# Kernel tuning notes

Hardware: AMD Instinct MI355X
Metric: run time of the kernel (lower is better)

## Reference

```python
import jax, jax.numpy as jnp
import numpy as np

N_NODES = 100000
N_EDGES = 1600000
F_IN = 128
HID = 64
N_CLASSES = 1
N_GRAPHS = 1024


def gcn_conv(x, src, dst, deg_inv_sqrt, W, b):
    # PyG GCNConv: out = D^{-1/2}(A+I)D^{-1/2} X W + b
    xw = x @ W  # [N, H]
    norm = deg_inv_sqrt[src] * deg_inv_sqrt[dst]  # [E]
    msg = xw[src] * norm[:, None]  # gather + scale
    agg = jax.ops.segment_sum(msg, dst, num_segments=N_NODES)
    # self-loop contribution: norm_ii = deg_inv_sqrt[i]^2
    agg = agg + xw * (deg_inv_sqrt ** 2)[:, None]
    return agg + b


def setup_inputs() -> dict:
    key = jax.random.key(0)
    ks = jax.random.split(key, 12)
    x = jax.random.normal(ks[0], (N_NODES, F_IN), dtype=jnp.float32)
    edge_index = jax.random.randint(ks[1], (2, N_EDGES), 0, N_NODES, dtype=jnp.int64)
    batch = jnp.sort(jax.random.randint(ks[2], (N_NODES,), 0, N_GRAPHS, dtype=jnp.int64))
    def glorot(k, fan_in, fan_out):
        s = (6.0 / (fan_in + fan_out)) ** 0.5
        return jax.random.uniform(k, (fan_in, fan_out), dtype=jnp.float32, minval=-s, maxval=s)
    W1 = glorot(ks[3], F_IN, HID); b1 = jnp.zeros((HID,), jnp.float32)
    W2 = glorot(ks[4], HID, HID); b2 = jnp.zeros((HID,), jnp.float32)
    W3 = glorot(ks[5], HID, HID); b3 = jnp.zeros((HID,), jnp.float32)
    Wl = glorot(ks[6], HID, N_CLASSES); bl = jnp.zeros((N_CLASSES,), jnp.float32)
    return {"x": x, "edge_index": edge_index, "batch": batch,
            "W1": W1, "b1": b1, "W2": W2, "b2": b2, "W3": W3, "b3": b3,
            "Wl": Wl, "bl": bl}


def reference(x, edge_index, batch, W1, b1, W2, b2, W3, b3, Wl, bl):
    src, dst = edge_index[0], edge_index[1]
    # degree with self-loops: deg[i] = (# incoming edges at i) + 1
    deg = jax.ops.segment_sum(jnp.ones((N_EDGES,), x.dtype), dst, num_segments=N_NODES) + 1.0
    deg_inv_sqrt = jax.lax.rsqrt(deg)
    h = jax.nn.relu(gcn_conv(x, src, dst, deg_inv_sqrt, W1, b1))
    # dropout: identity in eval mode
    h = jax.nn.relu(gcn_conv(h, src, dst, deg_inv_sqrt, W2, b2))
    h = gcn_conv(h, src, dst, deg_inv_sqrt, W3, b3)
    # global_mean_pool over graph ids
    sums = jax.ops.segment_sum(h, batch, num_segments=N_GRAPHS)
    counts = jax.ops.segment_sum(jnp.ones((N_NODES,), h.dtype), batch, num_segments=N_GRAPHS)
    pooled = sums / jnp.maximum(counts, 1.0)[:, None]  # [G, HID]
    return pooled @ Wl + bl  # [G, num_classes]
```

## Files before the change

### kernel.cpp

```cpp
#include <hip/hip_runtime.h>
#include <hip/hip_bf16.h>

#define N_NODES 100000
#define N_EDGES 1600000
#define F_IN 128
#define HID 64
#define N_GRAPHS 1024

#define SH 9
#define NBU 196
#define NB 200
#define BCAP 9728
#define EPB 2048
#define NSLICE 2

typedef __attribute__((ext_vector_type(8))) short bf16x8;
typedef __attribute__((ext_vector_type(4))) float f32x4;
typedef __attribute__((ext_vector_type(4))) unsigned int u32x4;

__device__ __forceinline__ unsigned short f2bf(float f) {
    __hip_bfloat16 h = __float2bfloat16(f);
    return *reinterpret_cast<unsigned short*>(&h);
}
__device__ __forceinline__ float bf2f(unsigned int u) {
    return __uint_as_float(u << 16);
}

__device__ __forceinline__ float loadf(const void* p, size_t i, int f32) {
    if (f32) return ((const float*)p)[i];
    return __bfloat162float(((const __hip_bfloat16*)p)[i]);
}
__device__ __forceinline__ int loadi(const void* p, size_t i, int i64) {
    if (i64) return (int)((const long long*)p)[i];
    return ((const int*)p)[i];
}

__global__ void k_init(const unsigned int* __restrict__ xw_,
                       const unsigned int* __restrict__ ei_,
                       int* __restrict__ flags,
                       int* __restrict__ gcnt, int* __restrict__ bcnt) {
    __shared__ int cnt_f, cnt_i;
    int t = threadIdx.x;
    if (t == 0) { cnt_f = 0; cnt_i = 0; }
    __syncthreads();
    unsigned int w = xw_[t];
    unsigned int e = (w >> 7) & 0xFFu;
    if (e >= 100u && e <= 140u) atomicAdd(&cnt_f, 1);
    unsigned int iw = ei_[2 * t + 1];
    if (iw == 0u) atomicAdd(&cnt_i, 1);
    for (int i = t; i < N_GRAPHS; i += 256) gcnt[i] = 0;
    for (int i = t; i < NB; i += 256) bcnt[i] = 0;
    __syncthreads();
    if (t == 0) {
        flags[0] = (cnt_f < 180) ? 1 : 0;
        flags[1] = (cnt_i >= 128) ? 1 : 0;
    }
}

__global__ __launch_bounds__(256) void k_part(const void* __restrict__ ei,
                                              const void* __restrict__ batch,
                                              int* __restrict__ bcnt,
                                              int* __restrict__ gcnt,
                                              unsigned int* __restrict__ packed,
                                              const int* __restrict__ flags) {
    int I64 = flags[1];
    __shared__ int hist[NB];
    __shared__ int base[NB];
    __shared__ int ghist[N_GRAPHS];
    __shared__ unsigned int elds[EPB];
    __shared__ unsigned char ebkt[EPB];
    int t = threadIdx.x;
    if (t < NB) hist[t] = 0;
    for (int i = t; i < N_GRAPHS; i += 256) ghist[i] = 0;
    __syncthreads();
    if (t < 128) {
        int n = blockIdx.x * 128 + t;
        if (n < N_NODES) atomicAdd(&ghist[loadi(batch, n, I64)], 1);
    }
    int e0 = blockIdx.x * EPB;
#pragma unroll 4
    for (int it = 0; it < EPB / 256; ++it) {
        int idx = it * 256 + t;
        int e = e0 + idx;
        unsigned int pv = 0u;
        unsigned char bk = 0xFFu;
        if (e < N_EDGES) {
            int sN = loadi(ei, e, I64);
            int d = loadi(ei, (size_t)N_EDGES + e, I64);
            bk = (unsigned char)(d >> SH);
            pv = ((unsigned int)sN << SH) | (unsigned int)(d & 511);
            atomicAdd(&hist[d >> SH], 1);
        }
        elds[idx] = pv;
        ebkt[idx] = bk;
    }
    __syncthreads();
    if (t < NB) {
        base[t] = hist[t] ? atomicAdd(&bcnt[t], hist[t]) : 0;
        hist[t] = 0;
    }
    for (int i = t; i < N_GRAPHS; i += 256)
        if (ghist[i]) atomicAdd(&gcnt[i], ghist[i]);
    __syncthreads();
#pragma unroll 4
    for (int it = 0; it < EPB / 256; ++it) {
        int idx = it * 256 + t;
        unsigned char bk = ebkt[idx];
        if (bk != 0xFFu) {
            unsigned int pv = elds[idx];
            int r = atomicAdd(&hist[bk], 1);
            int pos = base[bk] + r;
            if (pos < BCAP)
                packed[(size_t)bk * BCAP + pos] = pv;
        }
    }
}

__global__ __launch_bounds__(512) void k_csr(const unsigned int* __restrict__ packed,
                                             const int* __restrict__ bcnt,
                                             float* __restrict__ dis,
                                             int2* __restrict__ rp2,
                                             int* __restrict__ csr,
                                             const int* __restrict__ gcnt,
                                             int* __restrict__ gptr) {
    __shared__ int hist[512];
    __shared__ int offs[512];
    __shared__ int elds[BCAP];
    int b = blockIdx.x;
    int t = threadIdx.x;
    if (b == NBU) {
        int a = gcnt[2 * t], bq = gcnt[2 * t + 1];
        int ps = a + bq;
        hist[t] = ps;
        __syncthreads();
        for (int off = 1; off < 512; off <<= 1) {
            int x = (t >= off) ? hist[t - off] : 0;
            __syncthreads();
            hist[t] += x;
            __syncthreads();
        }
        int excl = hist[t] - ps;
        gptr[2 * t] = excl;
        gptr[2 * t + 1] = excl + a;
        if (t == 511) gptr[1024] = hist[511];
        return;
    }
    int n = bcnt[b]; if (n > BCAP) n = BCAP;
    hist[t] = 0;
    __syncthreads();
    const unsigned int* pb = packed + (size_t)b * BCAP;
    for (int i = t; i < n; i += 512)
        atomicAdd(&hist[pb[i] & 511u], 1);
    __syncthreads();
    int c = hist[t];
    offs[t] = c;
    __syncthreads();
    for (int off = 1; off < 512; off <<= 1) {
        int x = (t >= off) ? offs[t - off] : 0;
        __syncthreads();
        offs[t] += x;
        __syncthreads();
    }
    int excl = offs[t] - c;
    int node = (b << SH) + t;
    int base = b * BCAP;
    if (node < N_NODES) {
        dis[node] = rsqrtf((float)c + 1.0f);
        rp2[node] = make_int2(base + excl, base + excl + c);
    }
    __syncthreads();
    offs[t] = excl;
    __syncthreads();
    for (int i = t; i < n; i += 512) {
        unsigned int p = pb[i];
        int pos = atomicAdd(&offs[p & 511u], 1);
        if (pos < BCAP) elds[pos] = (int)(p >> SH);
    }
    __syncthreads();
    for (int i = t; i < n; i += 512)
        csr[base + i] = elds[i];
}

template <int K>
__global__ __launch_bounds__(256) void k_gemm(const void* __restrict__ x,
                                              const void* __restrict__ W,
                                              const float* __restrict__ dis,
                                              unsigned short* __restrict__ out,
                                              const int* __restrict__ flags,
                                              int x_is_f32) {
    int Wf32 = flags[0];
    int xF32 = (x_is_f32 < 0) ? Wf32 : x_is_f32;
    __shared__ unsigned short Wt[64][K + 8];
    __shared__ unsigned short xs[32][K + 8];
    int t = threadIdx.x;
    int wave = t >> 6, lane = t & 63;
    int quad = lane >> 4, l16 = lane & 15;

    for (int id = t; id < 64 * K; id += 256) {
        int k = id >> 6, n = id & 63;
        Wt[n][k] = f2bf(loadf(W, id, Wf32));
    }
    __syncthreads();

    bf16x8 bfrag[K / 32];
#pragma unroll
    for (int c = 0; c < K / 32; ++c)
        bfrag[c] = *reinterpret_cast<bf16x8*>(&Wt[wave * 16 + l16][c * 32 + quad * 8]);

    const int ngroups = (N_NODES + 31) / 32;
    for (int g = blockIdx.x; g < ngroups; g += gridDim.x) {
        __syncthreads();
        int row0 = g * 32;
        for (int cid = t; cid < 4 * K; cid += 256) {
            int rr = cid / (K / 8), c8 = cid % (K / 8);
            int r = row0 + rr;
            u32x4 val = {0u, 0u, 0u, 0u};
            if (r < N_NODES) {
                size_t base = (size_t)r * K + c8 * 8;
                if (xF32) {
                    const u32x4* xp = (const u32x4*)x;
                    u32x4 q0 = xp[base / 4];
                    u32x4 q1 = xp[base / 4 + 1];
                    val.x = f2bf(__uint_as_float(q0.x)) | ((unsigned int)f2bf(__uint_as_float(q0.y)) << 16);
                    val.y = f2bf(__uint_as_float(q0.z)) | ((unsigned int)f2bf(__uint_as_float(q0.w)) << 16);
                    val.z = f2bf(__uint_as_float(q1.x)) | ((unsigned int)f2bf(__uint_as_float(q1.y)) << 16);
                    val.w = f2bf(__uint_as_float(q1.z)) | ((unsigned int)f2bf(__uint_as_float(q1.w)) << 16);
                } else {
                    val = ((const u32x4*)x)[base / 8];
                }
            }
            *reinterpret_cast<u32x4*>(&xs[rr][c8 * 8]) = val;
        }
        __syncthreads();

        f32x4 acc0 = {0.f, 0.f, 0.f, 0.f};
        f32x4 acc1 = {0.f, 0.f, 0.f, 0.f};
#pragma unroll
        for (int c = 0; c < K / 32; ++c) {
            bf16x8 a0 = *reinterpret_cast<bf16x8*>(&xs[l16][c * 32 + quad * 8]);
            bf16x8 a1 = *reinterpret_cast<bf16x8*>(&xs[16 + l16][c * 32 + quad * 8]);
            acc0 = __builtin_amdgcn_mfma_f32_16x16x32_bf16(a0, bfrag[c], acc0, 0, 0, 0);
            acc1 = __builtin_amdgcn_mfma_f32_16x16x32_bf16(a1, bfrag[c], acc1, 0, 0, 0);
        }
        int col = wave * 16 + l16;
        unsigned short* ow = out + (size_t)(col >> 5) * (N_NODES * 32);
        int f = col & 31;
#pragma unroll
        for (int reg = 0; reg < 4; ++reg) {
            int r0 = row0 + quad * 4 + reg;
            if (r0 < N_NODES) ow[(size_t)r0 * 32 + f] = f2bf(acc0[reg] * dis[r0]);
            int r1 = row0 + 16 + quad * 4 + reg;
            if (r1 < N_NODES) ow[(size_t)r1 * 32 + f] = f2bf(acc1[reg] * dis[r1]);
        }
    }
}

__global__ __launch_bounds__(256) void k_gather_sm(const int2* __restrict__ rp2,
                                                   const int* __restrict__ csr,
                                                   const float* __restrict__ dis,
                                                   const unsigned short* __restrict__ xws,
                                                   const void* __restrict__ bias,
                                                   unsigned short* __restrict__ out,
                                                   const int* __restrict__ flags) {
    int F32 = flags[0];
    int blk = blockIdx.x;
    int xcd = blk & 7;
    int s = xcd >> 2;
    int grp = ((blk >> 3) << 2) | (xcd & 3);
    int wave = threadIdx.x >> 6, lane = threadIdx.x & 63;
    int nodesub = lane >> 4;
    int eslot = (lane >> 2) & 3;
    int q = lane & 3;
    const u32x4* xs4 = (const u32x4*)(xws + (size_t)s * N_NODES * 32);
    u32x4* op = (u32x4*)out;
    float bb0 = loadf(bias, s * 32 + q * 8 + 0, F32);
    float bb1 = loadf(bias, s * 32 + q * 8 + 1, F32);
    float bb2 = loadf(bias, s * 32 + q * 8 + 2, F32);
    float bb3 = loadf(bias, s * 32 + q * 8 + 3, F32);
    float bb4 = loadf(bias, s * 32 + q * 8 + 4, F32);
    float bb5 = loadf(bias, s * 32 + q * 8 + 5, F32);
    float bb6 = loadf(bias, s * 32 + q * 8 + 6, F32);
    float bb7 = loadf(bias, s * 32 + q * 8 + 7, F32);
    int wbase = grp * 64 + wave * 16;

    for (int ni = 0; ni < 4; ++ni) {
        int node = wbase + ni * 4 + nodesub;
        int valid = node < N_NODES;
        int2 se = valid ? rp2[node] : make_int2(0, 0);
        float a0 = 0.f, a1 = 0.f, a2 = 0.f, a3 = 0.f;
        float a4 = 0.f, a5 = 0.f, a6 = 0.f, a7 = 0.f;
        int j = se.x + eslot;
        if (j < se.y) {
            int src = csr[j];
            u32x4 vc = xs4[(size_t)src * 4 + q];
            int jn = j + 4;
            int sn = (jn < se.y) ? csr[jn] : 0;
            while (jn < se.y) {
                u32x4 vn = xs4[(size_t)sn * 4 + q];
                int jn2 = jn + 4;
                int sn2 = (jn2 < se.y) ? csr[jn2] : 0;
                a0 += bf2f(vc.x & 0xFFFFu); a1 += bf2f(vc.x >> 16);
                a2 += bf2f(vc.y & 0xFFFFu); a3 += bf2f(vc.y >> 16);
                a4 += bf2f(vc.z & 0xFFFFu); a5 += bf2f(vc.z >> 16);
                a6 += bf2f(vc.w & 0xFFFFu); a7 += bf2f(vc.w >> 16);
                vc = vn; sn = sn2; jn = jn2;
            }
            a0 += bf2f(vc.x & 0xFFFFu); a1 += bf2f(vc.x >> 16);
            a2 += bf2f(vc.y & 0xFFFFu); a3 += bf2f(vc.y >> 16);
            a4 += bf2f(vc.z & 0xFFFFu); a5 += bf2f(vc.z >> 16);
            a6 += bf2f(vc.w & 0xFFFFu); a7 += bf2f(vc.w >> 16);
        }
#pragma unroll
        for (int off = 4; off <= 8; off <<= 1) {
            a0 += __shfl_down(a0, off, 64); a1 += __shfl_down(a1, off, 64);
            a2 += __shfl_down(a2, off, 64); a3 += __shfl_down(a3, off, 64);
            a4 += __shfl_down(a4, off, 64); a5 += __shfl_down(a5, off, 64);
            a6 += __shfl_down(a6, off, 64); a7 += __shfl_down(a7, off, 64);
        }
        if (((lane & 12) == 0) && valid) {
            u32x4 sv = xs4[(size_t)node * 4 + q];
            float dn = dis[node];
            float v0 = fmaf(a0 + bf2f(sv.x & 0xFFFFu), dn, bb0);
            float v1 = fmaf(a1 + bf2f(sv.x >> 16),     dn, bb1);
            float v2 = fmaf(a2 + bf2f(sv.y & 0xFFFFu), dn, bb2);
            float v3 = fmaf(a3 + bf2f(sv.y >> 16),     dn, bb3);
            float v4 = fmaf(a4 + bf2f(sv.z & 0xFFFFu), dn, bb4);
            float v5 = fmaf(a5 + bf2f(sv.z >> 16),     dn, bb5);
            float v6 = fmaf(a6 + bf2f(sv.w & 0xFFFFu), dn, bb6);
            float v7 = fmaf(a7 + bf2f(sv.w >> 16),     dn, bb7);
            v0 = fmaxf(v0, 0.f) * dn; v1 = fmaxf(v1, 0.f) * dn;
            v2 = fmaxf(v2, 0.f) * dn; v3 = fmaxf(v3, 0.f) * dn;
            v4 = fmaxf(v4, 0.f) * dn; v5 = fmaxf(v5, 0.f) * dn;
            v6 = fmaxf(v6, 0.f) * dn; v7 = fmaxf(v7, 0.f) * dn;
            u32x4 o;
            o.x = (unsigned int)f2bf(v0) | ((unsigned int)f2bf(v1) << 16);
            o.y = (unsigned int)f2bf(v2) | ((unsigned int)f2bf(v3) << 16);
            o.z = (unsigned int)f2bf(v4) | ((unsigned int)f2bf(v5) << 16);
            o.w = (unsigned int)f2bf(v6) | ((unsigned int)f2bf(v7) << 16);
            op[(size_t)node * 8 + s * 4 + q] = o;
        }
    }
}

__global__ __launch_bounds__(256) void k_fgl(const int2* __restrict__ rp2,
                                             const int* __restrict__ csr,
                                             const float* __restrict__ dis,
                                             const unsigned short* __restrict__ hs_in,
                                             const void* __restrict__ W,
                                             const void* __restrict__ bias,
                                             unsigned short* __restrict__ out,
                                             int relu_scale,
                                             const int* __restrict__ flags) {
    int F32 = flags[0];
    __shared__ unsigned short Wt[64][72];
    __shared__ unsigned short xs[64][72];
    int t = threadIdx.x;
    int w = t >> 6, lane = t & 63;
    for (int id = t; id < 64 * 64; id += 256) {
        int k = id >> 6, n = id & 63;
        Wt[n][k] = f2bf(loadf(W, id, F32));
    }
    int node2 = lane >> 5;
    int oct = lane & 7;
    const u32x4* xr = (const u32x4*)hs_in;
    int wbase = blockIdx.x * 64 + w * 16;
#pragma unroll
    for (int p = 0; p < 8; ++p) {
        int node = wbase + p * 2 + node2;
        int valid = node < N_NODES;
        int2 se = valid ? rp2[node] : make_int2(0, 0);
        float a0 = 0.f, a1 = 0.f, a2 = 0.f, a3 = 0.f;
        float a4 = 0.f, a5 = 0.f, a6 = 0.f, a7 = 0.f;
        int j = se.x + ((lane >> 3) & 3);
        if (j < se.y) {
            int src = csr[j];
            u32x4 vc = xr[(size_t)src * 8 + oct];
            int jn = j + 4;
            int sn = (jn < se.y) ? csr[jn] : 0;
            while (jn < se.y) {
                u32x4 vn = xr[(size_t)sn * 8 + oct];
                int jn2 = jn + 4;
                int sn2 = (jn2 < se.y) ? csr[jn2] : 0;
                a0 += bf2f(vc.x & 0xFFFFu); a1 += bf2f(vc.x >> 16);
                a2 += bf2f(vc.y & 0xFFFFu); a3 += bf2f(vc.y >> 16);
                a4 += bf2f(vc.z & 0xFFFFu); a5 += bf2f(vc.z >> 16);
                a6 += bf2f(vc.w & 0xFFFFu); a7 += bf2f(vc.w >> 16);
                vc = vn; sn = sn2; jn = jn2;
            }
            a0 += bf2f(vc.x & 0xFFFFu); a1 += bf2f(vc.x >> 16);
            a2 += bf2f(vc.y & 0xFFFFu); a3 += bf2f(vc.y >> 16);
            a4 += bf2f(vc.z & 0xFFFFu); a5 += bf2f(vc.z >> 16);
            a6 += bf2f(vc.w & 0xFFFFu); a7 += bf2f(vc.w >> 16);
        }
#pragma unroll
        for (int off = 8; off <= 16; off <<= 1) {
            a0 += __shfl_down(a0, off, 64); a1 += __shfl_down(a1, off, 64);
            a2 += __shfl_down(a2, off, 64); a3 += __shfl_down(a3, off, 64);
            a4 += __shfl_down(a4, off, 64); a5 += __shfl_down(a5, off, 64);
            a6 += __shfl_down(a6, off, 64); a7 += __shfl_down(a7, off, 64);
        }
        if ((lane & 24) == 0) {
            u32x4 sv = {0u, 0u, 0u, 0u};
            float dn = 0.f;
            if (valid) { sv = xr[(size_t)node * 8 + oct]; dn = dis[node]; }
            float v0 = (a0 + bf2f(sv.x & 0xFFFFu)) * dn;
            float v1 = (a1 + bf2f(sv.x >> 16))     * dn;
            float v2 = (a2 + bf2f(sv.y & 0xFFFFu)) * dn;
            float v3 = (a3 + bf2f(sv.y >> 16))     * dn;
            float v4 = (a4 + bf2f(sv.z & 0xFFFFu)) * dn;
            float v5 = (a5 + bf2f(sv.z >> 16))     * dn;
            float v6 = (a6 + bf2f(sv.w & 0xFFFFu)) * dn;
            float v7 = (a7 + bf2f(sv.w >> 16))     * dn;
            u32x4 o;
            o.x = (unsigned int)f2bf(v0) | ((unsigned int)f2bf(v1) << 16);
            o.y = (unsigned int)f2bf(v2) | ((unsigned int)f2bf(v3) << 16);
            o.z = (unsigned int)f2bf(v4) | ((unsigned int)f2bf(v5) << 16);
            o.w = (unsigned int)f2bf(v6) | ((unsigned int)f2bf(v7) << 16);
            *reinterpret_cast<u32x4*>(&xs[w * 16 + p * 2 + node2][oct * 8]) = o;
        }
    }
    __syncthreads();
    int quad = lane >> 4, l16 = lane & 15;
    bf16x8 bfrag[2];
#pragma unroll
    for (int c = 0; c < 2; ++c)
        bfrag[c] = *reinterpret_cast<bf16x8*>(&Wt[w * 16 + l16][c * 32 + quad * 8]);
    f32x4 acc[4];
#pragma unroll
    for (int rg = 0; rg < 4; ++rg) acc[rg] = (f32x4){0.f, 0.f, 0.f, 0.f};
#pragma unroll
    for (int c = 0; c < 2; ++c) {
#pragma unroll
        for (int rg = 0; rg < 4; ++rg) {
            bf16x8 a = *reinterpret_cast<bf16x8*>(&xs[rg * 16 + l16][c * 32 + quad * 8]);
            acc[rg] = __builtin_amdgcn_mfma_f32_16x16x32_bf16(a, bfrag[c], acc[rg], 0, 0, 0);
        }
    }
    int col = w * 16 + l16;
    float bcol = loadf(bias, col, F32);
    int rbase = blockIdx.x * 64;
#pragma unroll
    for (int rg = 0; rg < 4; ++rg) {
#pragma unroll
        for (int reg = 0; reg < 4; ++reg) {
            int row = rbase + rg * 16 + quad * 4 + reg;
            if (row < N_NODES) {
                float v = acc[rg][reg] + bcol;
                if (relu_scale) v = fmaxf(v, 0.f) * dis[row];
                out[(size_t)row * 64 + col] = f2bf(v);
            }
        }
    }
}

__global__ __launch_bounds__(256) void k_pool3(const int* __restrict__ gptr,
                                               const int2* __restrict__ rp2,
                                               const int* __restrict__ csr,
                                               const float* __restrict__ dis,
                                               const unsigned short* __restrict__ hs,
                                               const void* __restrict__ W3,
                                               const void* __restrict__ b3,
                                               const void* __restrict__ Wl,
                                               const void* __restrict__ bl,
                                               void* __restrict__ out,
                                               const int* __restrict__ flags) {
    int F32 = flags[0];
    __shared__ float w3l[64];
    __shared__ float part[4];
    __shared__ float cterm;
    int t = threadIdx.x;
    if (t < 64) {
        float acc = 0.f;
        for (int k = 0; k < 64; ++k)
            acc += loadf(W3, t * 64 + k, F32) * loadf(Wl, k, F32);
        w3l[t] = acc;
    }
    if (t == 64) {
        float acc = 0.f;
        for (int k = 0; k < 64; ++k)
            acc += loadf(b3, k, F32) * loadf(Wl, k, F32);
        cterm = acc;
    }
    __syncthreads();
    int g = blockIdx.x;
    int w = t >> 6, lane = t & 63;
    int eslot = lane >> 3, oct = lane & 7;
    int s0 = gptr[g], e0 = gptr[g + 1];
    const u32x4* xr = (const u32x4*)hs;
    float P0 = 0.f, P1 = 0.f, P2 = 0.f, P3 = 0.f;
    float P4 = 0.f, P5 = 0.f, P6 = 0.f, P7 = 0.f;
    for (int node = s0 + w; node < e0; node += 4) {
        int2 se = rp2[node];
        float t0 = 0.f, t1 = 0.f, t2 = 0.f, t3 = 0.f;
        float t4 = 0.f, t5 = 0.f, t6 = 0.f, t7 = 0.f;
        int j = se.x + eslot;
        if (j < se.y) {
            int src = csr[j];
            u32x4 vc = xr[(size_t)src * 8 + oct];
            int jn = j + 8;
            int sn = (jn < se.y) ? csr[jn] : 0;
            while (jn < se.y) {
                u32x4 vn = xr[(size_t)sn * 8 + oct];
                int jn2 = jn + 8;
                int sn2 = (jn2 < se.y) ? csr[jn2] : 0;
                t0 += bf2f(vc.x & 0xFFFFu); t1 += bf2f(vc.x >> 16);
                t2 += bf2f(vc.y & 0xFFFFu); t3 += bf2f(vc.y >> 16);
                t4 += bf2f(vc.z & 0xFFFFu); t5 += bf2f(vc.z >> 16);
                t6 += bf2f(vc.w & 0xFFFFu); t7 += bf2f(vc.w >> 16);
                vc = vn; sn = sn2; jn = jn2;
            }
            t0 += bf2f(vc.x & 0xFFFFu); t1 += bf2f(vc.x >> 16);
            t2 += bf2f(vc.y & 0xFFFFu); t3 += bf2f(vc.y >> 16);
            t4 += bf2f(vc.z & 0xFFFFu); t5 += bf2f(vc.z >> 16);
            t6 += bf2f(vc.w & 0xFFFFu); t7 += bf2f(vc.w >> 16);
        }
        if (eslot == 0) {
            u32x4 sv = xr[(size_t)node * 8 + oct];
            t0 += bf2f(sv.x & 0xFFFFu); t1 += bf2f(sv.x >> 16);
            t2 += bf2f(sv.y & 0xFFFFu); t3 += bf2f(sv.y >> 16);
            t4 += bf2f(sv.z & 0xFFFFu); t5 += bf2f(sv.z >> 16);
            t6 += bf2f(sv.w & 0xFFFFu); t7 += bf2f(sv.w >> 16);
        }
        float dn = dis[node];
        P0 = fmaf(t0, dn, P0); P1 = fmaf(t1, dn, P1);
        P2 = fmaf(t2, dn, P2); P3 = fmaf(t3, dn, P3);
        P4 = fmaf(t4, dn, P4); P5 = fmaf(t5, dn, P5);
        P6 = fmaf(t6, dn, P6); P7 = fmaf(t7, dn, P7);
    }
#pragma unroll
    for (int off = 8; off <= 32; off <<= 1) {
        P0 += __shfl_down(P0, off, 64); P1 += __shfl_down(P1, off, 64);
        P2 += __shfl_down(P2, off, 64); P3 += __shfl_down(P3, off, 64);
        P4 += __shfl_down(P4, off, 64); P5 += __shfl_down(P5, off, 64);
        P6 += __shfl_down(P6, off, 64); P7 += __shfl_down(P7, off, 64);
    }
    float v = 0.f;
    if (eslot == 0) {
        int f = oct * 8;
        v = P0 * w3l[f] + P1 * w3l[f + 1] + P2 * w3l[f + 2] + P3 * w3l[f + 3]
          + P4 * w3l[f + 4] + P5 * w3l[f + 5] + P6 * w3l[f + 6] + P7 * w3l[f + 7];
    }
    v += __shfl_down(v, 4, 64);
    v += __shfl_down(v, 2, 64);
    v += __shfl_down(v, 1, 64);
    if (lane == 0) part[w] = v;
    __syncthreads();
    if (t == 0) {
        float cnt = fmaxf((float)(e0 - s0), 1.0f);
        float r = (part[0] + part[1] + part[2] + part[3]) / cnt
                + ((e0 > s0) ? cterm : 0.f) + loadf(bl, 0, F32);
        if (F32) ((float*)out)[g] = r;
        else     ((__hip_bfloat16*)out)[g] = __float2bfloat16(r);
    }
}

extern "C" void kernel_launch(void* const* d_in, const int* in_sizes, int n_in,
                              void* d_out, int out_size, void* d_ws, size_t ws_size,
                              hipStream_t stream) {
    const void* x     = d_in[0];
    const void* ei    = d_in[1];
    const void* batch = d_in[2];
    const void* W1 = d_in[3];
    const void* b1 = d_in[4];
    const void* W2 = d_in[5];
    const void* b2 = d_in[6];
    const void* W3 = d_in[7];
    const void* b3 = d_in[8];
    const void* Wl = d_in[9];
    const void* bl = d_in[10];

    float* dis   = (float*)d_ws;
    int2*  rp2   = (int2*)(dis + 100352);
    int*   csr   = (int*)(rp2 + 100352);
    int*   gcnt  = csr + NB * BCAP;
    int*   gptr  = gcnt + 1024;
    int*   bcnt  = gptr + 1056;
    int*   flags = bcnt + 256;
    unsigned int* packed = (unsigned int*)(flags + 16);
    unsigned short* bufA = (unsigned short*)(packed + (size_t)NB * BCAP);
    unsigned short* bufB = bufA + (size_t)N_NODES * 64;

    const int TB = 256;
    dim3 blk(TB);
    int gGA = 391 * 8;
    int gFG = (N_NODES + 63) / 64;

    k_init<<<1, blk, 0, stream>>>((const unsigned int*)x, (const unsigned int*)ei,
                                  flags, gcnt, bcnt);
    k_part<<<(N_EDGES + EPB - 1) / EPB, blk, 0, stream>>>(ei, batch, bcnt, gcnt, packed, flags);
    k_csr<<<NBU + 1, 512, 0, stream>>>(packed, bcnt, dis, rp2, csr, gcnt, gptr);

    k_gemm<F_IN><<<1024, blk, 0, stream>>>(x, W1, dis, bufA, flags, -1);
    k_gather_sm<<<gGA, blk, 0, stream>>>(rp2, csr, dis, bufA, b1, bufB, flags);
    k_fgl<<<gFG, blk, 0, stream>>>(rp2, csr, dis, bufB, W2, b2, bufA, 1, flags);
    k_pool3<<<N_GRAPHS, blk, 0, stream>>>(gptr, rp2, csr, dis, bufA,
                                          W3, b3, Wl, bl, d_out, flags);
}
```

Baseline: 342.3 us.

## Project layer-3 features to scalars before aggregation and pool with atomics

Layer 3 and the head are linear, so each node's 64-wide feature is first reduced to one scalar z = h·(W3·Wl). Aggregation then gathers scalars instead of 64-wide bf16 rows, and graph pooling uses float atomics into a per-graph accumulator. The W3·Wl product moves into the init kernel. This cuts layer-3 gather traffic by about 64x, at the cost of two extra launches and atomic contention on graph sums; atomic ordering also makes the float summation non-deterministic.

```diff
diff --git a/kernel.cpp b/kernel.cpp
--- a/kernel.cpp
+++ b/kernel.cpp
@@ -38,8 +38,11 @@
 __global__ void k_init(const unsigned int* __restrict__ xw_,
                        const unsigned int* __restrict__ ei_,
                        int* __restrict__ flags,
-                       int* __restrict__ gcnt, int* __restrict__ bcnt) {
-    __shared__ int cnt_f, cnt_i;
+                       int* __restrict__ gcnt, int* __restrict__ bcnt,
+                       const void* __restrict__ W3, const void* __restrict__ b3,
+                       const void* __restrict__ Wl,
+                       float* __restrict__ w3l, float* __restrict__ gacc) {
+    __shared__ int cnt_f, cnt_i, sF32;
     int t = threadIdx.x;
     if (t == 0) { cnt_f = 0; cnt_i = 0; }
     __syncthreads();
@@ -48,12 +51,28 @@
     if (e >= 100u && e <= 140u) atomicAdd(&cnt_f, 1);
     unsigned int iw = ei_[2 * t + 1];
     if (iw == 0u) atomicAdd(&cnt_i, 1);
-    for (int i = t; i < N_GRAPHS; i += 256) gcnt[i] = 0;
+    for (int i = t; i < N_GRAPHS; i += 256) { gcnt[i] = 0; gacc[i] = 0.f; }
     for (int i = t; i < NB; i += 256) bcnt[i] = 0;
     __syncthreads();
     if (t == 0) {
-        flags[0] = (cnt_f < 180) ? 1 : 0;
+        int f = (cnt_f < 180) ? 1 : 0;
+        flags[0] = f;
         flags[1] = (cnt_i >= 128) ? 1 : 0;
+        sF32 = f;
+    }
+    __syncthreads();
+    int F32 = sF32;
+    if (t < 64) {
+        float acc = 0.f;
+        for (int k = 0; k < 64; ++k)
+            acc += loadf(W3, t * 64 + k, F32) * loadf(Wl, k, F32);
+        w3l[t] = acc;
+    }
+    if (t == 64) {
+        float acc = 0.f;
+        for (int k = 0; k < 64; ++k)
+            acc += loadf(b3, k, F32) * loadf(Wl, k, F32);
+        w3l[64] = acc;
     }
 }
 
@@ -453,105 +472,67 @@
     }
 }
 
-__global__ __launch_bounds__(256) void k_pool3(const int* __restrict__ gptr,
-                                               const int2* __restrict__ rp2,
-                                               const int* __restrict__ csr,
-                                               const float* __restrict__ dis,
-                                               const unsigned short* __restrict__ hs,
-                                               const void* __restrict__ W3,
-                                               const void* __restrict__ b3,
-                                               const void* __restrict__ Wl,
-                                               const void* __restrict__ bl,
-                                               void* __restrict__ out,
-                                               const int* __restrict__ flags) {
+__global__ __launch_bounds__(256) void k_z(const unsigned short* __restrict__ hs,
+                                           const float* __restrict__ w3l,
+                                           float* __restrict__ z) {
+    __shared__ float w3s[64];
+    int t = threadIdx.x;
+    if (t < 64) w3s[t] = w3l[t];
+    __syncthreads();
+    int lane = t & 63, wave = t >> 6;
+    int rowsub = lane >> 3, oct = lane & 7;
+    int node = blockIdx.x * 32 + wave * 8 + rowsub;
+    const u32x4* xr = (const u32x4*)hs;
+    u32x4 v = xr[(size_t)node * 8 + oct];
+    int f = oct * 8;
+    float pd = bf2f(v.x & 0xFFFFu) * w3s[f + 0] + bf2f(v.x >> 16) * w3s[f + 1]
+             + bf2f(v.y & 0xFFFFu) * w3s[f + 2] + bf2f(v.y >> 16) * w3s[f + 3]
+             + bf2f(v.z & 0xFFFFu) * w3s[f + 4] + bf2f(v.z >> 16) * w3s[f + 5]
+             + bf2f(v.w & 0xFFFFu) * w3s[f + 6] + bf2f(v.w >> 16) * w3s[f + 7];
+    pd += __shfl_down(pd, 4, 64);
+    pd += __shfl_down(pd, 2, 64);
+    pd += __shfl_down(pd, 1, 64);
+    if (oct == 0) z[node] = pd;
+}
+
+__global__ __launch_bounds__(256) void k_l3(const int2* __restrict__ rp2,
+                                            const int* __restrict__ csr,
+                                            const float* __restrict__ dis,
+                                            const float* __restrict__ z,
+                                            const void* __restrict__ batch,
+                                            float* __restrict__ gacc,
+                                            const int* __restrict__ flags) {
+    int I64 = flags[1];
+    int node = blockIdx.x * 256 + threadIdx.x;
+    if (node >= N_NODES) return;
+    int2 se = rp2[node];
+    float sum = z[node];
+    int j = se.x;
+    if (j < se.y) {
+        int s = csr[j];
+        for (;;) {
+            int jn = j + 1;
+            int sn = (jn < se.y) ? csr[jn] : 0;
+            sum += z[s];
+            if (jn >= se.y) break;
+            j = jn; s = sn;
+        }
+    }
+    float y = dis[node] * sum;
+    unsafeAtomicAdd(&gacc[loadi(batch, node, I64)], y);
+}
+
+__global__ void k_head(const int* __restrict__ gptr, const float* __restrict__ gacc,
+                       const float* __restrict__ w3l, const void* __restrict__ bl,
+                       void* __restrict__ out, const int* __restrict__ flags) {
     int F32 = flags[0];
-    __shared__ float w3l[64];
-    __shared__ float part[4];
-    __shared__ float cterm;
-    int t = threadIdx.x;
-    if (t < 64) {
-        float acc = 0.f;
-        for (int k = 0; k < 64; ++k)
-            acc += loadf(W3, t * 64 + k, F32) * loadf(Wl, k, F32);
-        w3l[t] = acc;
-    }
-    if (t == 64) {
-        float acc = 0.f;
-        for (int k = 0; k < 64; ++k)
-            acc += loadf(b3, k, F32) * loadf(Wl, k, F32);
-        cterm = acc;
-    }
-    __syncthreads();
-    int g = blockIdx.x;
-    int w = t >> 6, lane = t & 63;
-    int eslot = lane >> 3, oct = lane & 7;
-    int s0 = gptr[g], e0 = gptr[g + 1];
-    const u32x4* xr = (const u32x4*)hs;
-    float P0 = 0.f, P1 = 0.f, P2 = 0.f, P3 = 0.f;
-    float P4 = 0.f, P5 = 0.f, P6 = 0.f, P7 = 0.f;
-    for (int node = s0 + w; node < e0; node += 4) {
-        int2 se = rp2[node];
-        float t0 = 0.f, t1 = 0.f, t2 = 0.f, t3 = 0.f;
-        float t4 = 0.f, t5 = 0.f, t6 = 0.f, t7 = 0.f;
-        int j = se.x + eslot;
-        if (j < se.y) {
-            int src = csr[j];
-            u32x4 vc = xr[(size_t)src * 8 + oct];
-            int jn = j + 8;
-            int sn = (jn < se.y) ? csr[jn] : 0;
-            while (jn < se.y) {
-                u32x4 vn = xr[(size_t)sn * 8 + oct];
-                int jn2 = jn + 8;
-                int sn2 = (jn2 < se.y) ? csr[jn2] : 0;
-                t0 += bf2f(vc.x & 0xFFFFu); t1 += bf2f(vc.x >> 16);
-                t2 += bf2f(vc.y & 0xFFFFu); t3 += bf2f(vc.y >> 16);
-                t4 += bf2f(vc.z & 0xFFFFu); t5 += bf2f(vc.z >> 16);
-                t6 += bf2f(vc.w & 0xFFFFu); t7 += bf2f(vc.w >> 16);
-                vc = vn; sn = sn2; jn = jn2;
-            }
-            t0 += bf2f(vc.x & 0xFFFFu); t1 += bf2f(vc.x >> 16);
-            t2 += bf2f(vc.y & 0xFFFFu); t3 += bf2f(vc.y >> 16);
-            t4 += bf2f(vc.z & 0xFFFFu); t5 += bf2f(vc.z >> 16);
-            t6 += bf2f(vc.w & 0xFFFFu); t7 += bf2f(vc.w >> 16);
-        }
-        if (eslot == 0) {
-            u32x4 sv = xr[(size_t)node * 8 + oct];
-            t0 += bf2f(sv.x & 0xFFFFu); t1 += bf2f(sv.x >> 16);
-            t2 += bf2f(sv.y & 0xFFFFu); t3 += bf2f(sv.y >> 16);
-            t4 += bf2f(sv.z & 0xFFFFu); t5 += bf2f(sv.z >> 16);
-            t6 += bf2f(sv.w & 0xFFFFu); t7 += bf2f(sv.w >> 16);
-        }
-        float dn = dis[node];
-        P0 = fmaf(t0, dn, P0); P1 = fmaf(t1, dn, P1);
-        P2 = fmaf(t2, dn, P2); P3 = fmaf(t3, dn, P3);
-        P4 = fmaf(t4, dn, P4); P5 = fmaf(t5, dn, P5);
-        P6 = fmaf(t6, dn, P6); P7 = fmaf(t7, dn, P7);
-    }
-#pragma unroll
-    for (int off = 8; off <= 32; off <<= 1) {
-        P0 += __shfl_down(P0, off, 64); P1 += __shfl_down(P1, off, 64);
-        P2 += __shfl_down(P2, off, 64); P3 += __shfl_down(P3, off, 64);
-        P4 += __shfl_down(P4, off, 64); P5 += __shfl_down(P5, off, 64);
-        P6 += __shfl_down(P6, off, 64); P7 += __shfl_down(P7, off, 64);
-    }
-    float v = 0.f;
-    if (eslot == 0) {
-        int f = oct * 8;
-        v = P0 * w3l[f] + P1 * w3l[f + 1] + P2 * w3l[f + 2] + P3 * w3l[f + 3]
-          + P4 * w3l[f + 4] + P5 * w3l[f + 5] + P6 * w3l[f + 6] + P7 * w3l[f + 7];
-    }
-    v += __shfl_down(v, 4, 64);
-    v += __shfl_down(v, 2, 64);
-    v += __shfl_down(v, 1, 64);
-    if (lane == 0) part[w] = v;
-    __syncthreads();
-    if (t == 0) {
-        float cnt = fmaxf((float)(e0 - s0), 1.0f);
-        float r = (part[0] + part[1] + part[2] + part[3]) / cnt
-                + ((e0 > s0) ? cterm : 0.f) + loadf(bl, 0, F32);
-        if (F32) ((float*)out)[g] = r;
-        else     ((__hip_bfloat16*)out)[g] = __float2bfloat16(r);
-    }
+    int g = blockIdx.x * 256 + threadIdx.x;
+    if (g >= N_GRAPHS) return;
+    int cnt = gptr[g + 1] - gptr[g];
+    float r = (cnt > 0) ? (gacc[g] / (float)cnt + w3l[64]) : 0.f;
+    r += loadf(bl, 0, F32);
+    if (F32) ((float*)out)[g] = r;
+    else     ((__hip_bfloat16*)out)[g] = __float2bfloat16(r);
 }
 
 extern "C" void kernel_launch(void* const* d_in, const int* in_sizes, int n_in,
@@ -576,7 +557,10 @@
     int*   gptr  = gcnt + 1024;
     int*   bcnt  = gptr + 1056;
     int*   flags = bcnt + 256;
-    unsigned int* packed = (unsigned int*)(flags + 16);
+    float* w3l   = (float*)(flags + 16);
+    float* gacc  = w3l + 80;
+    unsigned int* packed = (unsigned int*)(gacc + 1024);
+    float* z = (float*)packed;
     unsigned short* bufA = (unsigned short*)(packed + (size_t)NB * BCAP);
     unsigned short* bufB = bufA + (size_t)N_NODES * 64;
 
@@ -586,13 +570,14 @@
     int gFG = (N_NODES + 63) / 64;
 
     k_init<<<1, blk, 0, stream>>>((const unsigned int*)x, (const unsigned int*)ei,
-                                  flags, gcnt, bcnt);
+                                  flags, gcnt, bcnt, W3, b3, Wl, w3l, gacc);
     k_part<<<(N_EDGES + EPB - 1) / EPB, blk, 0, stream>>>(ei, batch, bcnt, gcnt, packed, flags);
     k_csr<<<NBU + 1, 512, 0, stream>>>(packed, bcnt, dis, rp2, csr, gcnt, gptr);
 
     k_gemm<F_IN><<<1024, blk, 0, stream>>>(x, W1, dis, bufA, flags, -1);
     k_gather_sm<<<gGA, blk, 0, stream>>>(rp2, csr, dis, bufA, b1, bufB, flags);
     k_fgl<<<gFG, blk, 0, stream>>>(rp2, csr, dis, bufB, W2, b2, bufA, 1, flags);
-    k_pool3<<<N_GRAPHS, blk, 0, stream>>>(gptr, rp2, csr, dis, bufA,
-                                          W3, b3, Wl, bl, d_out, flags);
-}
+    k_z<<<N_NODES / 32, blk, 0, stream>>>(bufA, w3l, z);
+    k_l3<<<(N_NODES + 255) / 256, blk, 0, stream>>>(rp2, csr, dis, z, batch, gacc, flags);
+    k_head<<<(N_GRAPHS + 255) / 256, blk, 0, stream>>>(gptr, gacc, w3l, bl, d_out, flags);
+}
```

After: 313.2 us. 8.5% less time.
